# Optimization experiments

Hardware: AMD Instinct MI355X
Metric: run time of the kernel (lower is better)

## Reference

```python
import jax, jax.numpy as jnp
import numpy as np

B, N, K = 4, 1024, 32
C_S, C_Z, C_H, H, PQ, PV = 384, 128, 16, 12, 4, 8
INF, EPS = 1e5, 1e-8
LN_EPS = 1e-5


def _quat_to_rot(q):
    # q: [..., 4] unit quaternions -> [..., 3, 3]
    w, x, y, z = q[..., 0], q[..., 1], q[..., 2], q[..., 3]
    r = jnp.stack([
        1 - 2 * (y * y + z * z), 2 * (x * y - w * z), 2 * (x * z + w * y),
        2 * (x * y + w * z), 1 - 2 * (x * x + z * z), 2 * (y * z - w * x),
        2 * (x * z - w * y), 2 * (y * z + w * x), 1 - 2 * (x * x + y * y),
    ], axis=-1)
    return r.reshape(q.shape[:-1] + (3, 3))


def _layernorm(x, scale, bias):
    m = jnp.mean(x, axis=-1, keepdims=True)
    v = jnp.mean((x - m) ** 2, axis=-1, keepdims=True)
    return (x - m) * jax.lax.rsqrt(v + LN_EPS) * scale + bias


def setup_inputs():
    key = jax.random.key(0)
    ks = jax.random.split(key, 16)
    s = jax.random.normal(ks[0], (B, N, C_S), jnp.float32)
    z = jax.random.normal(ks[1], (B, N, K, C_Z), jnp.float32)
    edge_index = jax.random.randint(ks[2], (B, N, K), 0, N, jnp.int32)
    quat = jax.random.normal(ks[3], (B, N, 4), jnp.float32)
    rot = _quat_to_rot(quat / jnp.linalg.norm(quat, axis=-1, keepdims=True))
    trans = 10.0 * jax.random.normal(ks[4], (B, N, 3), jnp.float32)
    s_mask = jnp.ones((B, N), jnp.float32)
    sc_s, sc_z = C_S ** -0.5, C_Z ** -0.5
    return {
        "s": s, "z": z, "edge_index": edge_index, "rot": rot, "trans": trans,
        "s_mask": s_mask,
        "ln_s_scale": jnp.ones((C_S,), jnp.float32),
        "ln_s_bias": jnp.zeros((C_S,), jnp.float32),
        "ln_z_scale": jnp.ones((C_Z,), jnp.float32),
        "ln_z_bias": jnp.zeros((C_Z,), jnp.float32),
        "w_q": sc_s * jax.random.normal(ks[5], (C_S, H * C_H), jnp.float32),
        "w_k": sc_s * jax.random.normal(ks[6], (C_S, H * C_H), jnp.float32),
        "w_v": sc_s * jax.random.normal(ks[7], (C_S, H * C_H), jnp.float32),
        "w_q_pts": sc_s * jax.random.normal(ks[8], (C_S, H * PQ * 3), jnp.float32),
        "w_kv_pts": sc_s * jax.random.normal(ks[9], (C_S, H * (PQ + PV) * 3), jnp.float32),
        "w_b": sc_z * jax.random.normal(ks[10], (C_Z, H), jnp.float32),
        "w_down_z": sc_z * jax.random.normal(ks[11], (C_Z, C_Z // 4), jnp.float32),
        "head_weights": jnp.full((H,), 0.541324854612918, jnp.float32),  # softplus^-1(1)
        "w_out": (H * 80) ** -0.5 * jax.random.normal(ks[12], (H * (C_Z // 4 + C_H + PV * 4), C_S), jnp.float32),
    }


def reference(s, z, edge_index, rot, trans, s_mask, ln_s_scale, ln_s_bias,
              ln_z_scale, ln_z_bias, w_q, w_k, w_v, w_q_pts, w_kv_pts, w_b,
              w_down_z, head_weights, w_out):
    bidx = jnp.arange(B)[:, None, None]
    s_ln = _layernorm(s, ln_s_scale, ln_s_bias)          # [B,N,C_S]
    z_ln = _layernorm(z, ln_z_scale, ln_z_bias)          # [B,N,K,C_Z]

    q = (s_ln @ w_q).reshape(B, N, H, C_H)
    k = (s_ln @ w_k)[bidx, edge_index].reshape(B, N, K, H, C_H)
    v = (s_ln @ w_v)[bidx, edge_index].reshape(B, N, K, H, C_H)

    # query points in global frame (query residue's rigid)
    q_pts = (s_ln @ w_q_pts).reshape(B, N, H * PQ, 3)
    q_pts = jnp.einsum('bnij,bnpj->bnpi', rot, q_pts) + trans[:, :, None]
    q_pts = q_pts.reshape(B, N, H, PQ, 3)

    # kv points: gather neighbor local points, then (as in source) apply the
    # QUERY residue's rigid r[..., None, None]
    kv = (s_ln @ w_kv_pts)[bidx, edge_index].reshape(B, N, K, H * (PQ + PV), 3)
    kv = jnp.einsum('bnij,bnkpj->bnkpi', rot, kv) + trans[:, :, None, None]
    kv = kv.reshape(B, N, K, H, PQ + PV, 3)
    k_pts, v_pts = kv[..., :PQ, :], kv[..., PQ:, :]

    b_bias = z_ln @ w_b                                   # [B,N,K,H]
    a = jnp.einsum('bnhc,bnkhc->bnkh', q, k) * (1.0 / (3 * C_H)) ** 0.5
    a = a + (1.0 / 3.0) ** 0.5 * b_bias

    disp = q_pts[:, :, None] - k_pts                      # [B,N,K,H,PQ,3]
    sq = jnp.sum(disp * disp, axis=-1)                    # [B,N,K,H,PQ]
    hw = jax.nn.softplus(head_weights) * (1.0 / (3 * (PQ * 9.0 / 2))) ** 0.5
    a = a - 0.5 * jnp.sum(sq * hw[:, None], axis=-1)      # [B,N,K,H]

    m = s_mask[:, :, None] * s_mask[bidx, edge_index]     # [B,N,K]
    a = a + (INF * (m - 1.0))[..., None]

    a = jax.nn.softmax(jnp.swapaxes(a, -1, -2), axis=-1)  # [B,N,H,K]

    o = jnp.einsum('bnhk,bnkhc->bnhc', a, v).reshape(B, N, H * C_H)

    o_pt = jnp.einsum('bnhk,bnkhvc->bnhvc', a, v_pts)     # [B,N,H,PV,3]
    o_pt = jnp.einsum('bnji,bnhvj->bnhvi', rot, o_pt - trans[:, :, None, None])
    dists = jnp.sqrt(jnp.sum(o_pt * o_pt, axis=-1) + EPS).reshape(B, N, H * PV)
    o_pt_flat = o_pt.reshape(B, N, H * PV * 3)

    o_pair = jnp.einsum('bnhk,bnkc->bnhc', a, z_ln @ w_down_z).reshape(B, N, -1)

    out = jnp.concatenate([o, o_pt_flat, dists, o_pair], axis=-1) @ w_out
    return out
```

## Files before the change

kernel.cpp:

```cpp
#include <hip/hip_runtime.h>
#include <hip/hip_bf16.h>
#include <hip/hip_cooperative_groups.h>

namespace cg = cooperative_groups;

constexpr int Bb = 4, Nn = 1024, Kk = 32;
constexpr int CS = 384, CZ = 128, CH = 16, Hh = 12, PQn = 4, PVn = 8;
constexpr int NCOLS = 1152;
constexpr int FEAT = 960;
constexpr int NNODE = Bb * Nn;
constexpr int NEDGE = NNODE * Kk;
constexpr int ZOC = 44;
constexpr int NPREP = 1728 + 1440 + 1024 + 1;

constexpr int O_WZP   = 4;
constexpr int O_BVEC  = O_WZP + 6144;
constexpr int O_CSUM  = O_BVEC + 48;
constexpr int O_P     = O_CSUM + 48;
constexpr int O_ZOUT  = O_P + NNODE * NCOLS;
constexpr int O_SLNH  = O_ZOUT + NEDGE * ZOC;
constexpr int O_SLNL  = O_SLNH + NNODE * CS / 2;
constexpr int O_WNTH  = O_SLNL + NNODE * CS / 2;
constexpr int O_WNTL  = O_WNTH + NCOLS * CS / 2;
constexpr int O_WOTH  = O_WNTL + NCOLS * CS / 2;
constexpr int O_WOTL  = O_WOTH + CS * FEAT / 2;
constexpr int O_FEATH = O_SLNH;
constexpr int O_FEATL = O_WOTL + CS * FEAT / 2;
constexpr int TOTAL_F = O_FEATL + NNODE * FEAT / 2;

typedef __attribute__((ext_vector_type(8)))  short short8x;
typedef __attribute__((ext_vector_type(16))) float f32x16;

__device__ __forceinline__ float ldf(const float* p, int i) { return p[i]; }
__device__ __forceinline__ float ldf(const __hip_bfloat16* p, int i) { return __bfloat162float(p[i]); }
__device__ __forceinline__ void stf(float* p, size_t i, float v) { p[i] = v; }
__device__ __forceinline__ void stf(__hip_bfloat16* p, size_t i, float v) { p[i] = __float2bfloat16(v); }
__device__ __forceinline__ float4 ld4(const float* p, size_t i) { return *(const float4*)(p + i); }
__device__ __forceinline__ float4 ld4(const __hip_bfloat16* p, size_t i) {
    ushort4 u = *(const ushort4*)(p + i);
    return make_float4(__uint_as_float((unsigned)u.x << 16),
                       __uint_as_float((unsigned)u.y << 16),
                       __uint_as_float((unsigned)u.z << 16),
                       __uint_as_float((unsigned)u.w << 16));
}
__device__ __forceinline__ void split_bf(float v, unsigned short& h, unsigned short& l) {
    h = (unsigned short)(__float_as_uint(v) >> 16);
    float r = v - __uint_as_float((unsigned)h << 16);
    l = (unsigned short)(__float_as_uint(r) >> 16);
}

__global__ void k_detect(const unsigned* smask_raw, int* flag) {
    if (threadIdx.x == 0) *flag = (smask_raw[0] == 0x3F803F80u) ? 1 : 0;
}

template <typename T>
__device__ __forceinline__ void dev_prep(int vb, int t,
    const T* s, const T* lns_sc, const T* lns_bi,
    const T* wq, const T* wk, const T* wv, const T* wqp, const T* wkvp, const T* wout,
    const T* wb, const T* wdz, const T* zsc, const T* zbi, float* wsf)
{
    unsigned short* wntH = (unsigned short*)(wsf + O_WNTH);
    unsigned short* wntL = (unsigned short*)(wsf + O_WNTL);
    unsigned short* wotH = (unsigned short*)(wsf + O_WOTH);
    unsigned short* wotL = (unsigned short*)(wsf + O_WOTL);
    unsigned short* slnH = (unsigned short*)(wsf + O_SLNH);
    unsigned short* slnL = (unsigned short*)(wsf + O_SLNL);
    if (vb < 1728) {
        int idx = vb * 256 + t;
        int n = idx / 384, k = idx - n * 384;
        float v;
        if      (n < 192) v = ldf(wq,  k * 192 + n);
        else if (n < 384) v = ldf(wk,  k * 192 + n - 192);
        else if (n < 576) v = ldf(wv,  k * 192 + n - 384);
        else if (n < 720) v = ldf(wqp, k * 144 + n - 576);
        else              v = ldf(wkvp, k * 432 + n - 720);
        unsigned short h, l; split_bf(v, h, l);
        wntH[n * 384 + k] = h; wntL[n * 384 + k] = l;
    } else if (vb < 3168) {
        int idx = (vb - 1728) * 256 + t;
        int n = idx / 960, k = idx - n * 960;
        float v = ldf(wout, k * 384 + n);
        unsigned short h, l; split_bf(v, h, l);
        wotH[n * 960 + k] = h; wotL[n * 960 + k] = l;
    } else if (vb < 4192) {
        int row = (vb - 3168) * 4 + (t >> 6), lane = t & 63;
        float x[6]; float sum = 0, sq = 0;
        #pragma unroll
        for (int j = 0; j < 6; j++) {
            float v = ldf(s, row * CS + lane + 64 * j);
            x[j] = v; sum += v; sq += v * v;
        }
        #pragma unroll
        for (int m = 32; m; m >>= 1) { sum += __shfl_xor(sum, m, 64); sq += __shfl_xor(sq, m, 64); }
        float mean = sum * (1.f / CS);
        float var  = sq * (1.f / CS) - mean * mean;
        float r = rsqrtf(var + 1e-5f);
        #pragma unroll
        for (int j = 0; j < 6; j++) {
            int c = lane + 64 * j;
            float y = (x[j] - mean) * r * ldf(lns_sc, c) + ldf(lns_bi, c);
            unsigned short h, l; split_bf(y, h, l);
            slnH[(size_t)row * CS + c] = h; slnL[(size_t)row * CS + c] = l;
        }
    } else {
        if (t < 128) {
            float sc = ldf(zsc, t);
            for (int o = 0; o < 48; o++) {
                float w = 0.f;
                if (o < 12)      w = ldf(wb, t * 12 + o);
                else if (o < 44) w = ldf(wdz, t * 32 + o - 12);
                wsf[O_WZP + t * 48 + o] = sc * w;
            }
        } else if (t < 176) {
            int o = t - 128;
            float acc = 0.f;
            if (o < 44)
                for (int c = 0; c < 128; c++)
                    acc += ldf(zbi, c) * (o < 12 ? ldf(wb, c * 12 + o) : ldf(wdz, c * 32 + o - 12));
            wsf[O_BVEC + o] = acc;
        } else if (t < 224) {
            int o = t - 176;
            float acc = 0.f;
            if (o < 44)
                for (int c = 0; c < 128; c++)
                    acc += ldf(zsc, c) * (o < 12 ? ldf(wb, c * 12 + o) : ldf(wdz, c * 32 + o - 12));
            wsf[O_CSUM + o] = acc;
        }
    }
}

template <typename T>
__device__ void dev_zg(int vb, int t, const T* z, const float* wzp, const float* bvec,
                       const float* csum, float* zout, float* sm)
{
    float* Ws  = sm;
    float* Asf = sm + 6144;
    float* mus = sm + 6144 + 2112;
    float* rss = mus + 128;
    int edge0 = vb * 128;
    for (int i = t; i < 6144; i += 256) Ws[i] = wzp[i];
    int sr = t >> 1, q = t & 1;
    int r0 = (t >> 2) * 2, col = (t & 3) * 12;
    float psum = 0, psq = 0;
    float acc[2][12] = {};
    for (int kt = 0; kt < CZ; kt += 16) {
        float4 z0 = ld4(z, (size_t)(edge0 + sr) * CZ + kt + q * 8);
        float4 z1 = ld4(z, (size_t)(edge0 + sr) * CZ + kt + q * 8 + 4);
        psum += z0.x + z0.y + z0.z + z0.w + z1.x + z1.y + z1.z + z1.w;
        psq  += z0.x*z0.x + z0.y*z0.y + z0.z*z0.z + z0.w*z0.w
              + z1.x*z1.x + z1.y*z1.y + z1.z*z1.z + z1.w*z1.w;
        __syncthreads();
        Asf[(q * 8 + 0) * 132 + sr] = z0.x;
        Asf[(q * 8 + 1) * 132 + sr] = z0.y;
        Asf[(q * 8 + 2) * 132 + sr] = z0.z;
        Asf[(q * 8 + 3) * 132 + sr] = z0.w;
        Asf[(q * 8 + 4) * 132 + sr] = z1.x;
        Asf[(q * 8 + 5) * 132 + sr] = z1.y;
        Asf[(q * 8 + 6) * 132 + sr] = z1.z;
        Asf[(q * 8 + 7) * 132 + sr] = z1.w;
        __syncthreads();
        #pragma unroll
        for (int kk = 0; kk < 16; kk++) {
            float a0 = Asf[kk * 132 + r0], a1 = Asf[kk * 132 + r0 + 1];
            const float* wr = &Ws[(kt + kk) * 48 + col];
            float4 b0 = *(const float4*)(wr);
            float4 b1 = *(const float4*)(wr + 4);
            float4 b2 = *(const float4*)(wr + 8);
            float bv[12] = {b0.x,b0.y,b0.z,b0.w,b1.x,b1.y,b1.z,b1.w,b2.x,b2.y,b2.z,b2.w};
            #pragma unroll
            for (int j = 0; j < 12; j++) { acc[0][j] += a0 * bv[j]; acc[1][j] += a1 * bv[j]; }
        }
    }
    psum += __shfl_xor(psum, 1, 64);
    psq  += __shfl_xor(psq, 1, 64);
    if (q == 0) {
        float mu = psum * (1.f / CZ);
        mus[sr] = mu;
        rss[sr] = rsqrtf(psq * (1.f / CZ) - mu * mu + 1e-5f);
    }
    __syncthreads();
    #pragma unroll
    for (int i = 0; i < 2; i++) {
        int r = r0 + i;
        float mu = mus[r], rs = rss[r];
        size_t e = edge0 + r;
        #pragma unroll
        for (int j = 0; j < 12; j++) {
            int c = col + j;
            if (c < ZOC) zout[e * ZOC + c] = rs * acc[i][j] - rs * mu * csum[c] + bvec[c];
        }
    }
    __syncthreads();
}

#define MFMA3(C, AH, AL, BH, BL)                                              \
    C = __builtin_amdgcn_mfma_f32_32x32x16_bf16(AH, BH, C, 0, 0, 0);          \
    C = __builtin_amdgcn_mfma_f32_32x32x16_bf16(AH, BL, C, 0, 0, 0);          \
    C = __builtin_amdgcn_mfma_f32_32x32x16_bf16(AL, BH, C, 0, 0, 0);

template <typename TO>
__device__ void dev_mgemm_tile(int bx, int by, int l,
                               const unsigned short* AH, const unsigned short* AL, int lda,
                               const unsigned short* BH, const unsigned short* BL, int ldb,
                               TO* C, int ldc, int Kdim)
{
    int r = l & 31, g = l >> 5;
    size_t a0 = (size_t)(bx * 64 + r) * lda + 8 * g;
    size_t a1 = a0 + (size_t)32 * lda;
    size_t b0 = (size_t)(by * 64 + r) * ldb + 8 * g;
    size_t b1 = b0 + (size_t)32 * ldb;
    f32x16 c00 = {}, c01 = {}, c10 = {}, c11 = {};
    for (int kt = 0; kt < Kdim; kt += 16) {
        short8x aH0 = *(const short8x*)(AH + a0 + kt), aH1 = *(const short8x*)(AH + a1 + kt);
        short8x aL0 = *(const short8x*)(AL + a0 + kt), aL1 = *(const short8x*)(AL + a1 + kt);
        short8x bH0 = *(const short8x*)(BH + b0 + kt), bH1 = *(const short8x*)(BH + b1 + kt);
        short8x bL0 = *(const short8x*)(BL + b0 + kt), bL1 = *(const short8x*)(BL + b1 + kt);
        MFMA3(c00, aH0, aL0, bH0, bL0)
        MFMA3(c01, aH0, aL0, bH1, bL1)
        MFMA3(c10, aH1, aL1, bH0, bL0)
        MFMA3(c11, aH1, aL1, bH1, bL1)
    }
    #pragma unroll
    for (int reg = 0; reg < 16; reg++) {
        int row = (reg & 3) + 8 * (reg >> 2) + 4 * g;
        size_t rm = (size_t)(bx * 64 + row);
        int cn = by * 64 + r;
        stf(C, rm * ldc + cn,             c00[reg]);
        stf(C, rm * ldc + cn + 32,        c01[reg]);
        stf(C, (rm + 32) * ldc + cn,      c10[reg]);
        stf(C, (rm + 32) * ldc + cn + 32, c11[reg]);
    }
}

template <typename T>
__device__ void dev_attn(int bid, int t, float* smAll, int* jsAll,
                         const float* P, const float* zout, const int* eidx,
                         const T* smask, const T* rot, const T* hwq,
                         unsigned short* featH, unsigned short* featL)
{
    int nb = ((bid & 7) << 7) + (bid >> 3);
    int w = t >> 6, lane = t & 63;
    int node = nb * 4 + w;
    int b = node >> 10;
    float* S = smAll + w * 1760;
    int* J = jsAll + w * 32;
    const float* Pn = P + (size_t)node * NCOLS;
    for (int u = lane; u < 336; u += 64)
        S[u] = (u < 192) ? Pn[u] : Pn[384 + u];
    if (lane < 32) {
        int j = eidx[node * Kk + lane];
        J[lane] = b * Nn + j;
        S[360 + lane] = ldf(smask, node) * ldf(smask, b * Nn + j);
    } else if (lane < 44) {
        int h = lane - 32;
        float x = ldf(hwq, h);
        S[336 + h] = logf(1.f + expf(x)) * 0.13608276348795434f;
    } else if (lane < 53) {
        int u = lane - 44;
        int i = u / 3, jj = u - i * 3;
        float m = 0;
        #pragma unroll
        for (int l2 = 0; l2 < 3; l2++)
            m += ldf(rot, node * 9 + l2 * 3 + i) * ldf(rot, node * 9 + l2 * 3 + jj);
        S[348 + u] = m;
    }
    __builtin_amdgcn_wave_barrier();
    #pragma unroll
    for (int it = 0; it < 6; it++) {
        int u = lane + 64 * it;
        int h = u >> 5, k = u & 31;
        const float* Pj = P + (size_t)J[k] * NCOLS;
        float qk = 0;
        const float4* pk4 = (const float4*)(Pj + 192 + h * 16);
        const float4* qs4 = (const float4*)(S + h * 16);
        #pragma unroll
        for (int c4 = 0; c4 < 4; c4++) {
            float4 pv = pk4[c4], qv = qs4[c4];
            qk += qv.x * pv.x + qv.y * pv.y + qv.z * pv.z + qv.w * pv.w;
        }
        float M00 = S[348], M01 = S[349], M02 = S[350],
              M11 = S[352], M12 = S[353], M22 = S[356];
        const float4* pp4 = (const float4*)(Pj + 720 + h * 36);
        const float4* qp4 = (const float4*)(S + 192 + h * 12);
        float4 A0 = pp4[0], A1 = pp4[1], A2 = pp4[2];
        float4 B0 = qp4[0], B1 = qp4[1], B2 = qp4[2];
        float d[12] = {B0.x - A0.x, B0.y - A0.y, B0.z - A0.z, B0.w - A0.w,
                       B1.x - A1.x, B1.y - A1.y, B1.z - A1.z, B1.w - A1.w,
                       B2.x - A2.x, B2.y - A2.y, B2.z - A2.z, B2.w - A2.w};
        float sq = 0;
        #pragma unroll
        for (int p = 0; p < 4; p++) {
            float d0 = d[p * 3], d1 = d[p * 3 + 1], d2 = d[p * 3 + 2];
            sq += M00 * d0 * d0 + M11 * d1 * d1 + M22 * d2 * d2
                + 2.f * (M01 * d0 * d1 + M02 * d0 * d2 + M12 * d1 * d2);
        }
        float logit = qk * 0.14433756729740643f
                    + 0.5773502691896258f * zout[((size_t)node * Kk + k) * ZOC + h]
                    - 0.5f * S[336 + h] * sq
                    + 1e5f * (S[360 + k] - 1.f);
        float mx = logit;
        #pragma unroll
        for (int m = 16; m; m >>= 1) mx = fmaxf(mx, __shfl_xor(mx, m, 64));
        float e = expf(logit - mx);
        float ssum = e;
        #pragma unroll
        for (int m = 16; m; m >>= 1) ssum += __shfl_xor(ssum, m, 64);
        S[392 + h * 33 + k] = e / ssum;
    }
    __builtin_amdgcn_wave_barrier();
    for (int u = lane; u < 216; u += 64) {
        int h, off, fbase, pair = 0;
        if (u < 48)       { h = u >> 2; off = 384 + h * 16 + (u & 3) * 4; fbase = h * 16 + (u & 3) * 4; }
        else if (u < 120) { int v = u - 48;  h = v / 6; int q = v - h * 6;
                            off = 732 + h * 36 + q * 4; fbase = 192 + h * 24 + q * 4; }
        else              { int v = u - 120; h = v >> 3;
                            off = 12 + (v & 7) * 4; fbase = 576 + h * 32 + (v & 7) * 4; pair = 1; }
        float4 acc = {0.f, 0.f, 0.f, 0.f};
        const float* lrow = S + 392 + h * 33;
        if (!pair) {
            #pragma unroll 8
            for (int k = 0; k < 32; k++) {
                float lw = lrow[k];
                float4 pv = *(const float4*)(P + (size_t)J[k] * NCOLS + off);
                acc.x += lw * pv.x; acc.y += lw * pv.y; acc.z += lw * pv.z; acc.w += lw * pv.w;
            }
        } else {
            const float* zr = zout + (size_t)node * Kk * ZOC + off;
            #pragma unroll 8
            for (int k = 0; k < 32; k++) {
                float lw = lrow[k];
                float4 pv = *(const float4*)(zr + k * ZOC);
                acc.x += lw * pv.x; acc.y += lw * pv.y; acc.z += lw * pv.z; acc.w += lw * pv.w;
            }
        }
        *(float4*)&S[788 + fbase] = acc;
    }
    __builtin_amdgcn_wave_barrier();
    for (int u = lane; u < 96; u += 64) {
        float r0 = S[788 + 192 + u * 3 + 0];
        float r1 = S[788 + 192 + u * 3 + 1];
        float r2 = S[788 + 192 + u * 3 + 2];
        float o0 = S[348] * r0 + S[349] * r1 + S[350] * r2;
        float o1 = S[351] * r0 + S[352] * r1 + S[353] * r2;
        float o2 = S[354] * r0 + S[355] * r1 + S[356] * r2;
        S[788 + 192 + u * 3 + 0] = o0;
        S[788 + 192 + u * 3 + 1] = o1;
        S[788 + 192 + u * 3 + 2] = o2;
        S[788 + 480 + u] = sqrtf(o0 * o0 + o1 * o1 + o2 * o2 + 1e-8f);
    }
    __builtin_amdgcn_wave_barrier();
    for (int u = lane; u < FEAT; u += 64) {
        unsigned short h, l; split_bf(S[788 + u], h, l);
        featH[(size_t)node * FEAT + u] = h;
        featL[(size_t)node * FEAT + u] = l;
    }
}

template <typename T, typename TO>
__global__ __launch_bounds__(256, 4) void k_fused(const T* s, const T* z, const int* eidx,
    const T* rot, const T* smask, const T* lns_sc, const T* lns_bi,
    const T* wq, const T* wk, const T* wv, const T* wqp, const T* wkvp,
    const T* wb, const T* wdz, const T* zsc, const T* zbi, const T* hwq, const T* wout,
    float* wsf, TO* out)
{
    __shared__ float sm[8512];
    __shared__ int js[4][32];
    cg::grid_group gg = cg::this_grid();
    int bid = blockIdx.x, t = threadIdx.x;

    for (int vb = bid; vb < NPREP; vb += 1024)
        dev_prep<T>(vb, t, s, lns_sc, lns_bi, wq, wk, wv, wqp, wkvp, wout, wb, wdz, zsc, zbi, wsf);
    gg.sync();

    dev_zg<T>(bid, t, z, wsf + O_WZP, wsf + O_BVEC, wsf + O_CSUM, wsf + O_ZOUT, sm);
    gg.sync();

    const unsigned short* slnH = (const unsigned short*)(wsf + O_SLNH);
    const unsigned short* slnL = (const unsigned short*)(wsf + O_SLNL);
    const unsigned short* wntH = (const unsigned short*)(wsf + O_WNTH);
    const unsigned short* wntL = (const unsigned short*)(wsf + O_WNTL);
    const unsigned short* wotH = (const unsigned short*)(wsf + O_WOTH);
    const unsigned short* wotL = (const unsigned short*)(wsf + O_WOTL);
    unsigned short* featH = (unsigned short*)(wsf + O_FEATH);
    unsigned short* featL = (unsigned short*)(wsf + O_FEATL);

    {
        int w = t >> 6, lane = t & 63;
        int wid = bid * 4 + w;
        for (int tile = wid; tile < 64 * 18; tile += 4096)
            dev_mgemm_tile<float>(tile & 63, tile >> 6, lane, slnH, slnL, CS, wntH, wntL, CS,
                                  wsf + O_P, NCOLS, CS);
    }
    gg.sync();

    dev_attn<T>(bid, t, sm, &js[0][0], wsf + O_P, wsf + O_ZOUT, eidx, smask, rot, hwq, featH, featL);
    gg.sync();

    {
        int w = t >> 6, lane = t & 63;
        int wid = bid * 4 + w;
        for (int tile = wid; tile < 64 * 6; tile += 4096)
            dev_mgemm_tile<TO>(tile & 63, tile >> 6, lane, featH, featL, FEAT, wotH, wotL, FEAT,
                               out, CS, FEAT);
    }
}

template <typename T>
__global__ __launch_bounds__(256) void k_prep_s(const T* s, const T* lns_sc, const T* lns_bi,
    const T* wq, const T* wk, const T* wv, const T* wqp, const T* wkvp, const T* wout,
    const T* wb, const T* wdz, const T* zsc, const T* zbi, float* wsf, const int* flag, int want) {
    if (flag && *flag != want) return;
    dev_prep<T>(blockIdx.x, threadIdx.x, s, lns_sc, lns_bi, wq, wk, wv, wqp, wkvp, wout,
                wb, wdz, zsc, zbi, wsf);
}

template <typename T>
__global__ __launch_bounds__(256) void k_zg_s(const T* z, const float* wzp, const float* bvec,
    const float* csum, float* zout, const int* flag, int want) {
    if (flag && *flag != want) return;
    __shared__ float sm[8512];
    dev_zg<T>(blockIdx.x, threadIdx.x, z, wzp, bvec, csum, zout, sm);
}

template <typename TO>
__global__ __launch_bounds__(64) void k_mgemm_s(const unsigned short* AH, const unsigned short* AL,
    int lda, const unsigned short* BH, const unsigned short* BL, int ldb,
    TO* C, int ldc, int Kdim, const int* flag, int want) {
    if (flag && *flag != want) return;
    dev_mgemm_tile<TO>(blockIdx.x, blockIdx.y, threadIdx.x, AH, AL, lda, BH, BL, ldb, C, ldc, Kdim);
}

template <typename T>
__global__ __launch_bounds__(256) void k_attn_s(const float* P, const float* zout, const int* eidx,
    const T* smask, const T* rot, const T* hwq, unsigned short* featH, unsigned short* featL,
    const int* flag, int want) {
    if (flag && *flag != want) return;
    __shared__ float sm[7040];
    __shared__ int js[4][32];
    dev_attn<T>(blockIdx.x, threadIdx.x, sm, &js[0][0], P, zout, eidx, smask, rot, hwq, featH, featL);
}

template <typename T, typename TO>
static void run_path(const void* s, const void* z, const int* eidx, const void* rot,
                     const void* smask, const void* lns_sc, const void* lns_bi,
                     const void* wq, const void* wk, const void* wv, const void* wqp,
                     const void* wkvp, const void* wb, const void* wdz, const void* zsc,
                     const void* zbi, const void* hwq, const void* wout,
                     float* wsf, void* dout, const int* fg, int want, bool try_coop,
                     hipStream_t stream)
{
    unsigned short* slnH = (unsigned short*)(wsf + O_SLNH);
    unsigned short* slnL = (unsigned short*)(wsf + O_SLNL);
    unsigned short* wntH = (unsigned short*)(wsf + O_WNTH);
    unsigned short* wntL = (unsigned short*)(wsf + O_WNTL);
    unsigned short* wotH = (unsigned short*)(wsf + O_WOTH);
    unsigned short* wotL = (unsigned short*)(wsf + O_WOTL);
    unsigned short* featH = (unsigned short*)(wsf + O_FEATH);
    unsigned short* featL = (unsigned short*)(wsf + O_FEATL);

    if (try_coop) {
        const T *sP = (const T*)s, *zP = (const T*)z, *rotP = (const T*)rot,
                *smP = (const T*)smask, *lsP = (const T*)lns_sc, *lbP = (const T*)lns_bi,
                *wqP = (const T*)wq, *wkP = (const T*)wk, *wvP = (const T*)wv,
                *wqpP = (const T*)wqp, *wkvpP = (const T*)wkvp, *wbP = (const T*)wb,
                *wdzP = (const T*)wdz, *zscP = (const T*)zsc, *zbiP = (const T*)zbi,
                *hwqP = (const T*)hwq, *woP = (const T*)wout;
        const int* eP = eidx;
        float* wsP = wsf;
        TO* oP = (TO*)dout;
        void* prm[20] = {&sP, &zP, &eP, &rotP, &smP, &lsP, &lbP, &wqP, &wkP, &wvP,
                         &wqpP, &wkvpP, &wbP, &wdzP, &zscP, &zbiP, &hwqP, &woP, &wsP, &oP};
        hipError_t err = hipLaunchCooperativeKernel(
            reinterpret_cast<void*>(&k_fused<T, TO>), dim3(1024), dim3(256), prm, 0, stream);
        if (err == hipSuccess) return;
        (void)hipGetLastError();
    }

    k_prep_s<T><<<NPREP, 256, 0, stream>>>((const T*)s, (const T*)lns_sc, (const T*)lns_bi,
        (const T*)wq, (const T*)wk, (const T*)wv, (const T*)wqp, (const T*)wkvp,
        (const T*)wout, (const T*)wb, (const T*)wdz, (const T*)zsc, (const T*)zbi, wsf, fg, want);
    k_zg_s<T><<<1024, 256, 0, stream>>>((const T*)z, wsf + O_WZP, wsf + O_BVEC, wsf + O_CSUM,
        wsf + O_ZOUT, fg, want);
    k_mgemm_s<float><<<dim3(64, 18), 64, 0, stream>>>(slnH, slnL, CS, wntH, wntL, CS,
        wsf + O_P, NCOLS, CS, (const int*)nullptr, 0);
    k_attn_s<T><<<1024, 256, 0, stream>>>(wsf + O_P, wsf + O_ZOUT, eidx, (const T*)smask,
        (const T*)rot, (const T*)hwq, featH, featL, fg, want);
    k_mgemm_s<TO><<<dim3(64, 6), 64, 0, stream>>>(featH, featL, FEAT, wotH, wotL, FEAT,
        (TO*)dout, CS, FEAT, fg, want);
}

extern "C" void kernel_launch(void* const* d_in, const int* in_sizes, int n_in,
                              void* d_out, int out_size, void* d_ws, size_t ws_size,
                              hipStream_t stream) {
    float* wsf = (float*)d_ws;
    int* flag = (int*)d_ws;
    const void* s = d_in[0];   const void* z = d_in[1];
    const int* eidx = (const int*)d_in[2];
    const void* rot = d_in[3];
    const void* smask = d_in[5];
    const void* lns_sc = d_in[6]; const void* lns_bi = d_in[7];
    const void* lnz_sc = d_in[8]; const void* lnz_bi = d_in[9];
    const void* wq = d_in[10]; const void* wk = d_in[11]; const void* wv = d_in[12];
    const void* wqp = d_in[13]; const void* wkvp = d_in[14];
    const void* wb = d_in[15]; const void* wdz = d_in[16];
    const void* hwq = d_in[17]; const void* wout = d_in[18];

    int mode = -1;
    if (in_sizes) {
        if (in_sizes[0] == NNODE * CS * 4) mode = 0;
        else if (in_sizes[0] == NNODE * CS * 2) mode = 1;
    }

    if (mode == 0) {
        run_path<float, float>(s, z, eidx, rot, smask, lns_sc, lns_bi, wq, wk, wv, wqp, wkvp,
                               wb, wdz, lnz_sc, lnz_bi, hwq, wout, wsf, d_out,
                               nullptr, 0, true, stream);
    } else if (mode == 1) {
        run_path<__hip_bfloat16, __hip_bfloat16>(s, z, eidx, rot, smask, lns_sc, lns_bi,
                               wq, wk, wv, wqp, wkvp, wb, wdz, lnz_sc, lnz_bi, hwq, wout,
                               wsf, d_out, nullptr, 0, true, stream);
    } else {
        k_detect<<<1, 64, 0, stream>>>((const unsigned*)smask, flag);
        run_path<float, float>(s, z, eidx, rot, smask, lns_sc, lns_bi, wq, wk, wv, wqp, wkvp,
                               wb, wdz, lnz_sc, lnz_bi, hwq, wout, wsf, d_out,
                               flag, 0, false, stream);
        run_path<__hip_bfloat16, __hip_bfloat16>(s, z, eidx, rot, smask, lns_sc, lns_bi,
                               wq, wk, wv, wqp, wkvp, wb, wdz, lnz_sc, lnz_bi, hwq, wout,
                               wsf, d_out, flag, 1, false, stream);
    }
}
```

Measured before the change: 405.2 us.

## Replace cooperative fused kernel with separate launches and restructured zg/attn kernels

Removes the cooperative single-kernel path with grid syncs and always launches five separate kernels. The z projection kernel now gives each thread a whole edge row with register accumulators, instead of a shared-memory tiled 2x12 micro-GEMM. The attention kernel now runs one 128-thread block per node instead of four nodes per 256-thread block. It writes split-bf16 features directly instead of staging all of them in shared memory. This drops the grid-barrier cost and raises per-kernel occupancy, at the cost of extra launch overhead and uncoalesced per-thread row loads of z.

```diff
diff --git a/kernel.cpp b/kernel.cpp
--- a/kernel.cpp
+++ b/kernel.cpp
@@ -1,8 +1,5 @@
 #include <hip/hip_runtime.h>
 #include <hip/hip_bf16.h>
-#include <hip/hip_cooperative_groups.h>
-
-namespace cg = cooperative_groups;
 
 constexpr int Bb = 4, Nn = 1024, Kk = 32;
 constexpr int CS = 384, CZ = 128, CH = 16, Hh = 12, PQn = 4, PVn = 8;
@@ -54,11 +51,13 @@
 }
 
 template <typename T>
-__device__ __forceinline__ void dev_prep(int vb, int t,
-    const T* s, const T* lns_sc, const T* lns_bi,
+__global__ __launch_bounds__(256) void k_prep_s(const T* s, const T* lns_sc, const T* lns_bi,
     const T* wq, const T* wk, const T* wv, const T* wqp, const T* wkvp, const T* wout,
-    const T* wb, const T* wdz, const T* zsc, const T* zbi, float* wsf)
+    const T* wb, const T* wdz, const T* zsc, const T* zbi, float* wsf,
+    const int* flag, int want)
 {
+    if (flag && *flag != want) return;
+    int vb = blockIdx.x, t = threadIdx.x;
     unsigned short* wntH = (unsigned short*)(wsf + O_WNTH);
     unsigned short* wntL = (unsigned short*)(wsf + O_WNTL);
     unsigned short* wotH = (unsigned short*)(wsf + O_WOTH);
@@ -130,67 +129,54 @@
 }
 
 template <typename T>
-__device__ void dev_zg(int vb, int t, const T* z, const float* wzp, const float* bvec,
-                       const float* csum, float* zout, float* sm)
+__global__ __launch_bounds__(256) void k_zg2(const T* z, const float* wzp, const float* bvec,
+                                             const float* csum, float* zout,
+                                             const int* flag, int want)
 {
-    float* Ws  = sm;
-    float* Asf = sm + 6144;
-    float* mus = sm + 6144 + 2112;
-    float* rss = mus + 128;
-    int edge0 = vb * 128;
+    if (flag && *flag != want) return;
+    __shared__ float Ws[6144];
+    __shared__ float BC[96];
+    int t = threadIdx.x;
     for (int i = t; i < 6144; i += 256) Ws[i] = wzp[i];
-    int sr = t >> 1, q = t & 1;
-    int r0 = (t >> 2) * 2, col = (t & 3) * 12;
-    float psum = 0, psq = 0;
-    float acc[2][12] = {};
-    for (int kt = 0; kt < CZ; kt += 16) {
-        float4 z0 = ld4(z, (size_t)(edge0 + sr) * CZ + kt + q * 8);
-        float4 z1 = ld4(z, (size_t)(edge0 + sr) * CZ + kt + q * 8 + 4);
-        psum += z0.x + z0.y + z0.z + z0.w + z1.x + z1.y + z1.z + z1.w;
-        psq  += z0.x*z0.x + z0.y*z0.y + z0.z*z0.z + z0.w*z0.w
-              + z1.x*z1.x + z1.y*z1.y + z1.z*z1.z + z1.w*z1.w;
-        __syncthreads();
-        Asf[(q * 8 + 0) * 132 + sr] = z0.x;
-        Asf[(q * 8 + 1) * 132 + sr] = z0.y;
-        Asf[(q * 8 + 2) * 132 + sr] = z0.z;
-        Asf[(q * 8 + 3) * 132 + sr] = z0.w;
-        Asf[(q * 8 + 4) * 132 + sr] = z1.x;
-        Asf[(q * 8 + 5) * 132 + sr] = z1.y;
-        Asf[(q * 8 + 6) * 132 + sr] = z1.z;
-        Asf[(q * 8 + 7) * 132 + sr] = z1.w;
-        __syncthreads();
-        #pragma unroll
-        for (int kk = 0; kk < 16; kk++) {
-            float a0 = Asf[kk * 132 + r0], a1 = Asf[kk * 132 + r0 + 1];
-            const float* wr = &Ws[(kt + kk) * 48 + col];
-            float4 b0 = *(const float4*)(wr);
-            float4 b1 = *(const float4*)(wr + 4);
-            float4 b2 = *(const float4*)(wr + 8);
-            float bv[12] = {b0.x,b0.y,b0.z,b0.w,b1.x,b1.y,b1.z,b1.w,b2.x,b2.y,b2.z,b2.w};
+    if (t < 48) { BC[t] = bvec[t]; BC[48 + t] = csum[t]; }
+    __syncthreads();
+    size_t e = (size_t)blockIdx.x * 256 + t;
+    float4 acc4[11];
+    #pragma unroll
+    for (int i = 0; i < 11; i++) acc4[i] = make_float4(0.f, 0.f, 0.f, 0.f);
+    float sum = 0.f, sq = 0.f;
+    for (int c = 0; c < CZ; c += 4) {
+        float4 zv = ld4(z, e * CZ + c);
+        sum += zv.x + zv.y + zv.z + zv.w;
+        sq  += zv.x * zv.x + zv.y * zv.y + zv.z * zv.z + zv.w * zv.w;
+        float zz[4] = {zv.x, zv.y, zv.z, zv.w};
+        #pragma unroll
+        for (int j = 0; j < 4; j++) {
+            const float4* wr = (const float4*)&Ws[(c + j) * 48];
+            float zc = zz[j];
             #pragma unroll
-            for (int j = 0; j < 12; j++) { acc[0][j] += a0 * bv[j]; acc[1][j] += a1 * bv[j]; }
-        }
-    }
-    psum += __shfl_xor(psum, 1, 64);
-    psq  += __shfl_xor(psq, 1, 64);
-    if (q == 0) {
-        float mu = psum * (1.f / CZ);
-        mus[sr] = mu;
-        rss[sr] = rsqrtf(psq * (1.f / CZ) - mu * mu + 1e-5f);
-    }
-    __syncthreads();
+            for (int i = 0; i < 11; i++) {
+                float4 w = wr[i];
+                acc4[i].x += zc * w.x; acc4[i].y += zc * w.y;
+                acc4[i].z += zc * w.z; acc4[i].w += zc * w.w;
+            }
+        }
+    }
+    float mu = sum * (1.f / CZ);
+    float rs = rsqrtf(sq * (1.f / CZ) - mu * mu + 1e-5f);
+    float* zr = zout + e * ZOC;
     #pragma unroll
-    for (int i = 0; i < 2; i++) {
-        int r = r0 + i;
-        float mu = mus[r], rs = rss[r];
-        size_t e = edge0 + r;
-        #pragma unroll
-        for (int j = 0; j < 12; j++) {
-            int c = col + j;
-            if (c < ZOC) zout[e * ZOC + c] = rs * acc[i][j] - rs * mu * csum[c] + bvec[c];
-        }
-    }
-    __syncthreads();
+    for (int i = 0; i < 11; i++) {
+        float4 a = acc4[i];
+        float4 bv = *(const float4*)&BC[i * 4];
+        float4 cs = *(const float4*)&BC[48 + i * 4];
+        float4 o;
+        o.x = rs * a.x - rs * mu * cs.x + bv.x;
+        o.y = rs * a.y - rs * mu * cs.y + bv.y;
+        o.z = rs * a.z - rs * mu * cs.z + bv.z;
+        o.w = rs * a.w - rs * mu * cs.w + bv.w;
+        *(float4*)(zr + i * 4) = o;
+    }
 }
 
 #define MFMA3(C, AH, AL, BH, BL)                                              \
@@ -199,12 +185,13 @@
     C = __builtin_amdgcn_mfma_f32_32x32x16_bf16(AL, BH, C, 0, 0, 0);
 
 template <typename TO>
-__device__ void dev_mgemm_tile(int bx, int by, int l,
-                               const unsigned short* AH, const unsigned short* AL, int lda,
-                               const unsigned short* BH, const unsigned short* BL, int ldb,
-                               TO* C, int ldc, int Kdim)
+__global__ __launch_bounds__(64) void k_mgemm_s(const unsigned short* AH, const unsigned short* AL,
+    int lda, const unsigned short* BH, const unsigned short* BL, int ldb,
+    TO* C, int ldc, int Kdim, const int* flag, int want)
 {
-    int r = l & 31, g = l >> 5;
+    if (flag && *flag != want) return;
+    int bx = blockIdx.x, by = blockIdx.y;
+    int l = threadIdx.x, r = l & 31, g = l >> 5;
     size_t a0 = (size_t)(bx * 64 + r) * lda + 8 * g;
     size_t a1 = a0 + (size_t)32 * lda;
     size_t b0 = (size_t)(by * 64 + r) * ldb + 8 * g;
@@ -233,30 +220,29 @@
 }
 
 template <typename T>
-__device__ void dev_attn(int bid, int t, float* smAll, int* jsAll,
-                         const float* P, const float* zout, const int* eidx,
-                         const T* smask, const T* rot, const T* hwq,
-                         unsigned short* featH, unsigned short* featL)
+__global__ __launch_bounds__(128, 8) void k_attn2(const float* P, const float* zout,
+    const int* eidx, const T* smask, const T* rot, const T* hwq,
+    unsigned short* featH, unsigned short* featL, const int* flag, int want)
 {
-    int nb = ((bid & 7) << 7) + (bid >> 3);
-    int w = t >> 6, lane = t & 63;
-    int node = nb * 4 + w;
+    if (flag && *flag != want) return;
+    __shared__ float S[1088];
+    __shared__ int J[32];
+    int bid = blockIdx.x, t = threadIdx.x;
+    int node = ((bid & 7) << 9) + (bid >> 3);
     int b = node >> 10;
-    float* S = smAll + w * 1760;
-    int* J = jsAll + w * 32;
     const float* Pn = P + (size_t)node * NCOLS;
-    for (int u = lane; u < 336; u += 64)
+    for (int u = t; u < 336; u += 128)
         S[u] = (u < 192) ? Pn[u] : Pn[384 + u];
-    if (lane < 32) {
-        int j = eidx[node * Kk + lane];
-        J[lane] = b * Nn + j;
-        S[360 + lane] = ldf(smask, node) * ldf(smask, b * Nn + j);
-    } else if (lane < 44) {
-        int h = lane - 32;
+    if (t < 32) {
+        int j = eidx[node * Kk + t];
+        J[t] = b * Nn + j;
+        S[360 + t] = ldf(smask, node) * ldf(smask, b * Nn + j);
+    } else if (t < 44) {
+        int h = t - 32;
         float x = ldf(hwq, h);
         S[336 + h] = logf(1.f + expf(x)) * 0.13608276348795434f;
-    } else if (lane < 53) {
-        int u = lane - 44;
+    } else if (t < 53) {
+        int u = t - 44;
         int i = u / 3, jj = u - i * 3;
         float m = 0;
         #pragma unroll
@@ -264,10 +250,10 @@
             m += ldf(rot, node * 9 + l2 * 3 + i) * ldf(rot, node * 9 + l2 * 3 + jj);
         S[348 + u] = m;
     }
-    __builtin_amdgcn_wave_barrier();
+    __syncthreads();
     #pragma unroll
-    for (int it = 0; it < 6; it++) {
-        int u = lane + 64 * it;
+    for (int it = 0; it < 3; it++) {
+        int u = t + 128 * it;
         int h = u >> 5, k = u & 31;
         const float* Pj = P + (size_t)J[k] * NCOLS;
         float qk = 0;
@@ -307,8 +293,9 @@
         for (int m = 16; m; m >>= 1) ssum += __shfl_xor(ssum, m, 64);
         S[392 + h * 33 + k] = e / ssum;
     }
-    __builtin_amdgcn_wave_barrier();
-    for (int u = lane; u < 216; u += 64) {
+    __syncthreads();
+    size_t fb = (size_t)node * FEAT;
+    for (int u = t; u < 216; u += 128) {
         int h, off, fbase, pair = 0;
         if (u < 48)       { h = u >> 2; off = 384 + h * 16 + (u & 3) * 4; fbase = h * 16 + (u & 3) * 4; }
         else if (u < 120) { int v = u - 48;  h = v / 6; int q = v - h * 6;
@@ -333,111 +320,31 @@
                 acc.x += lw * pv.x; acc.y += lw * pv.y; acc.z += lw * pv.z; acc.w += lw * pv.w;
             }
         }
-        *(float4*)&S[788 + fbase] = acc;
-    }
-    __builtin_amdgcn_wave_barrier();
-    for (int u = lane; u < 96; u += 64) {
-        float r0 = S[788 + 192 + u * 3 + 0];
-        float r1 = S[788 + 192 + u * 3 + 1];
-        float r2 = S[788 + 192 + u * 3 + 2];
+        if (u >= 48 && u < 120) {
+            *(float4*)&S[788 + (fbase - 192)] = acc;
+        } else {
+            ushort4 hi, lo;
+            split_bf(acc.x, hi.x, lo.x); split_bf(acc.y, hi.y, lo.y);
+            split_bf(acc.z, hi.z, lo.z); split_bf(acc.w, hi.w, lo.w);
+            *(ushort4*)(featH + fb + fbase) = hi;
+            *(ushort4*)(featL + fb + fbase) = lo;
+        }
+    }
+    __syncthreads();
+    if (t < 96) {
+        float r0 = S[788 + t * 3 + 0];
+        float r1 = S[788 + t * 3 + 1];
+        float r2 = S[788 + t * 3 + 2];
         float o0 = S[348] * r0 + S[349] * r1 + S[350] * r2;
         float o1 = S[351] * r0 + S[352] * r1 + S[353] * r2;
         float o2 = S[354] * r0 + S[355] * r1 + S[356] * r2;
-        S[788 + 192 + u * 3 + 0] = o0;
-        S[788 + 192 + u * 3 + 1] = o1;
-        S[788 + 192 + u * 3 + 2] = o2;
-        S[788 + 480 + u] = sqrtf(o0 * o0 + o1 * o1 + o2 * o2 + 1e-8f);
-    }
-    __builtin_amdgcn_wave_barrier();
-    for (int u = lane; u < FEAT; u += 64) {
-        unsigned short h, l; split_bf(S[788 + u], h, l);
-        featH[(size_t)node * FEAT + u] = h;
-        featL[(size_t)node * FEAT + u] = l;
-    }
-}
-
-template <typename T, typename TO>
-__global__ __launch_bounds__(256, 4) void k_fused(const T* s, const T* z, const int* eidx,
-    const T* rot, const T* smask, const T* lns_sc, const T* lns_bi,
-    const T* wq, const T* wk, const T* wv, const T* wqp, const T* wkvp,
-    const T* wb, const T* wdz, const T* zsc, const T* zbi, const T* hwq, const T* wout,
-    float* wsf, TO* out)
-{
-    __shared__ float sm[8512];
-    __shared__ int js[4][32];
-    cg::grid_group gg = cg::this_grid();
-    int bid = blockIdx.x, t = threadIdx.x;
-
-    for (int vb = bid; vb < NPREP; vb += 1024)
-        dev_prep<T>(vb, t, s, lns_sc, lns_bi, wq, wk, wv, wqp, wkvp, wout, wb, wdz, zsc, zbi, wsf);
-    gg.sync();
-
-    dev_zg<T>(bid, t, z, wsf + O_WZP, wsf + O_BVEC, wsf + O_CSUM, wsf + O_ZOUT, sm);
-    gg.sync();
-
-    const unsigned short* slnH = (const unsigned short*)(wsf + O_SLNH);
-    const unsigned short* slnL = (const unsigned short*)(wsf + O_SLNL);
-    const unsigned short* wntH = (const unsigned short*)(wsf + O_WNTH);
-    const unsigned short* wntL = (const unsigned short*)(wsf + O_WNTL);
-    const unsigned short* wotH = (const unsigned short*)(wsf + O_WOTH);
-    const unsigned short* wotL = (const unsigned short*)(wsf + O_WOTL);
-    unsigned short* featH = (unsigned short*)(wsf + O_FEATH);
-    unsigned short* featL = (unsigned short*)(wsf + O_FEATL);
-
-    {
-        int w = t >> 6, lane = t & 63;
-        int wid = bid * 4 + w;
-        for (int tile = wid; tile < 64 * 18; tile += 4096)
-            dev_mgemm_tile<float>(tile & 63, tile >> 6, lane, slnH, slnL, CS, wntH, wntL, CS,
-                                  wsf + O_P, NCOLS, CS);
-    }
-    gg.sync();
-
-    dev_attn<T>(bid, t, sm, &js[0][0], wsf + O_P, wsf + O_ZOUT, eidx, smask, rot, hwq, featH, featL);
-    gg.sync();
-
-    {
-        int w = t >> 6, lane = t & 63;
-        int wid = bid * 4 + w;
-        for (int tile = wid; tile < 64 * 6; tile += 4096)
-            dev_mgemm_tile<TO>(tile & 63, tile >> 6, lane, featH, featL, FEAT, wotH, wotL, FEAT,
-                               out, CS, FEAT);
-    }
-}
-
-template <typename T>
-__global__ __launch_bounds__(256) void k_prep_s(const T* s, const T* lns_sc, const T* lns_bi,
-    const T* wq, const T* wk, const T* wv, const T* wqp, const T* wkvp, const T* wout,
-    const T* wb, const T* wdz, const T* zsc, const T* zbi, float* wsf, const int* flag, int want) {
-    if (flag && *flag != want) return;
-    dev_prep<T>(blockIdx.x, threadIdx.x, s, lns_sc, lns_bi, wq, wk, wv, wqp, wkvp, wout,
-                wb, wdz, zsc, zbi, wsf);
-}
-
-template <typename T>
-__global__ __launch_bounds__(256) void k_zg_s(const T* z, const float* wzp, const float* bvec,
-    const float* csum, float* zout, const int* flag, int want) {
-    if (flag && *flag != want) return;
-    __shared__ float sm[8512];
-    dev_zg<T>(blockIdx.x, threadIdx.x, z, wzp, bvec, csum, zout, sm);
-}
-
-template <typename TO>
-__global__ __launch_bounds__(64) void k_mgemm_s(const unsigned short* AH, const unsigned short* AL,
-    int lda, const unsigned short* BH, const unsigned short* BL, int ldb,
-    TO* C, int ldc, int Kdim, const int* flag, int want) {
-    if (flag && *flag != want) return;
-    dev_mgemm_tile<TO>(blockIdx.x, blockIdx.y, threadIdx.x, AH, AL, lda, BH, BL, ldb, C, ldc, Kdim);
-}
-
-template <typename T>
-__global__ __launch_bounds__(256) void k_attn_s(const float* P, const float* zout, const int* eidx,
-    const T* smask, const T* rot, const T* hwq, unsigned short* featH, unsigned short* featL,
-    const int* flag, int want) {
-    if (flag && *flag != want) return;
-    __shared__ float sm[7040];
-    __shared__ int js[4][32];
-    dev_attn<T>(blockIdx.x, threadIdx.x, sm, &js[0][0], P, zout, eidx, smask, rot, hwq, featH, featL);
+        unsigned short h, l;
+        split_bf(o0, h, l); featH[fb + 192 + t * 3 + 0] = h; featL[fb + 192 + t * 3 + 0] = l;
+        split_bf(o1, h, l); featH[fb + 192 + t * 3 + 1] = h; featL[fb + 192 + t * 3 + 1] = l;
+        split_bf(o2, h, l); featH[fb + 192 + t * 3 + 2] = h; featL[fb + 192 + t * 3 + 2] = l;
+        float dd = sqrtf(o0 * o0 + o1 * o1 + o2 * o2 + 1e-8f);
+        split_bf(dd, h, l); featH[fb + 480 + t] = h; featL[fb + 480 + t] = l;
+    }
 }
 
 template <typename T, typename TO>
@@ -446,8 +353,7 @@
                      const void* wq, const void* wk, const void* wv, const void* wqp,
                      const void* wkvp, const void* wb, const void* wdz, const void* zsc,
                      const void* zbi, const void* hwq, const void* wout,
-                     float* wsf, void* dout, const int* fg, int want, bool try_coop,
-                     hipStream_t stream)
+                     float* wsf, void* dout, const int* fg, int want, hipStream_t stream)
 {
     unsigned short* slnH = (unsigned short*)(wsf + O_SLNH);
     unsigned short* slnL = (unsigned short*)(wsf + O_SLNL);
@@ -458,32 +364,14 @@
     unsigned short* featH = (unsigned short*)(wsf + O_FEATH);
     unsigned short* featL = (unsigned short*)(wsf + O_FEATL);
 
-    if (try_coop) {
-        const T *sP = (const T*)s, *zP = (const T*)z, *rotP = (const T*)rot,
-                *smP = (const T*)smask, *lsP = (const T*)lns_sc, *lbP = (const T*)lns_bi,
-                *wqP = (const T*)wq, *wkP = (const T*)wk, *wvP = (const T*)wv,
-                *wqpP = (const T*)wqp, *wkvpP = (const T*)wkvp, *wbP = (const T*)wb,
-                *wdzP = (const T*)wdz, *zscP = (const T*)zsc, *zbiP = (const T*)zbi,
-                *hwqP = (const T*)hwq, *woP = (const T*)wout;
-        const int* eP = eidx;
-        float* wsP = wsf;
-        TO* oP = (TO*)dout;
-        void* prm[20] = {&sP, &zP, &eP, &rotP, &smP, &lsP, &lbP, &wqP, &wkP, &wvP,
-                         &wqpP, &wkvpP, &wbP, &wdzP, &zscP, &zbiP, &hwqP, &woP, &wsP, &oP};
-        hipError_t err = hipLaunchCooperativeKernel(
-            reinterpret_cast<void*>(&k_fused<T, TO>), dim3(1024), dim3(256), prm, 0, stream);
-        if (err == hipSuccess) return;
-        (void)hipGetLastError();
-    }
-
     k_prep_s<T><<<NPREP, 256, 0, stream>>>((const T*)s, (const T*)lns_sc, (const T*)lns_bi,
         (const T*)wq, (const T*)wk, (const T*)wv, (const T*)wqp, (const T*)wkvp,
         (const T*)wout, (const T*)wb, (const T*)wdz, (const T*)zsc, (const T*)zbi, wsf, fg, want);
-    k_zg_s<T><<<1024, 256, 0, stream>>>((const T*)z, wsf + O_WZP, wsf + O_BVEC, wsf + O_CSUM,
-        wsf + O_ZOUT, fg, want);
+    k_zg2<T><<<NEDGE / 256, 256, 0, stream>>>((const T*)z, wsf + O_WZP, wsf + O_BVEC,
+        wsf + O_CSUM, wsf + O_ZOUT, fg, want);
     k_mgemm_s<float><<<dim3(64, 18), 64, 0, stream>>>(slnH, slnL, CS, wntH, wntL, CS,
-        wsf + O_P, NCOLS, CS, (const int*)nullptr, 0);
-    k_attn_s<T><<<1024, 256, 0, stream>>>(wsf + O_P, wsf + O_ZOUT, eidx, (const T*)smask,
+        wsf + O_P, NCOLS, CS, fg, want);
+    k_attn2<T><<<NNODE, 128, 0, stream>>>(wsf + O_P, wsf + O_ZOUT, eidx, (const T*)smask,
         (const T*)rot, (const T*)hwq, featH, featL, fg, want);
     k_mgemm_s<TO><<<dim3(64, 6), 64, 0, stream>>>(featH, featL, FEAT, wotH, wotL, FEAT,
         (TO*)dout, CS, FEAT, fg, want);
@@ -514,18 +402,18 @@
     if (mode == 0) {
         run_path<float, float>(s, z, eidx, rot, smask, lns_sc, lns_bi, wq, wk, wv, wqp, wkvp,
                                wb, wdz, lnz_sc, lnz_bi, hwq, wout, wsf, d_out,
-                               nullptr, 0, true, stream);
+                               nullptr, 0, stream);
     } else if (mode == 1) {
         run_path<__hip_bfloat16, __hip_bfloat16>(s, z, eidx, rot, smask, lns_sc, lns_bi,
                                wq, wk, wv, wqp, wkvp, wb, wdz, lnz_sc, lnz_bi, hwq, wout,
-                               wsf, d_out, nullptr, 0, true, stream);
+                               wsf, d_out, nullptr, 0, stream);
     } else {
         k_detect<<<1, 64, 0, stream>>>((const unsigned*)smask, flag);
         run_path<float, float>(s, z, eidx, rot, smask, lns_sc, lns_bi, wq, wk, wv, wqp, wkvp,
                                wb, wdz, lnz_sc, lnz_bi, hwq, wout, wsf, d_out,
-                               flag, 0, false, stream);
+                               flag, 0, stream);
         run_path<__hip_bfloat16, __hip_bfloat16>(s, z, eidx, rot, smask, lns_sc, lns_bi,
                                wq, wk, wv, wqp, wkvp, wb, wdz, lnz_sc, lnz_bi, hwq, wout,
-                               wsf, d_out, flag, 1, false, stream);
-    }
-}
+                               wsf, d_out, flag, 1, stream);
+    }
+}
```

Result: faster. 337.0 us (-16.8%).
